# Kernel optimization log

Measured on AMD Instinct MI355X. Metric: run time of the kernel, lower is better.

## Reference

```python
import jax, jax.numpy as jnp
import numpy as np

T, B, I, H, O = 512, 64, 256, 512, 256

def setup_inputs() -> dict:
    key = jax.random.key(0)
    ks = jax.random.split(key, 7)
    s_ih = 1.0 / np.sqrt(H)
    return {
        "x": jax.random.normal(ks[0], (T, B, I), dtype=jnp.float32),
        "W_ih": jax.random.uniform(ks[1], (H, I), jnp.float32, -s_ih, s_ih),
        "W_hh": jax.random.uniform(ks[2], (H, H), jnp.float32, -s_ih, s_ih),
        "b_ih": jax.random.uniform(ks[3], (H,), jnp.float32, -s_ih, s_ih),
        "b_hh": jax.random.uniform(ks[4], (H,), jnp.float32, -s_ih, s_ih),
        "W_out": jax.random.uniform(ks[5], (O, H), jnp.float32, -s_ih, s_ih),
        "b_out": jax.random.uniform(ks[6], (O,), jnp.float32, -s_ih, s_ih),
    }

def reference(x, W_ih, W_hh, b_ih, b_hh, W_out, b_out):
    # Precompute input projection for all timesteps: [T, B, H]
    xp = jnp.einsum('tbi,hi->tbh', x, W_ih) + b_ih + b_hh

    def step(h, xp_t):
        h_new = jnp.tanh(xp_t + h @ W_hh.T)
        return h_new, h_new

    h0 = jnp.zeros((x.shape[1], W_hh.shape[0]), dtype=x.dtype)
    h_last, rnn_out = jax.lax.scan(step, h0, xp)  # rnn_out: [T, B, H]
    y = jnp.einsum('tbh,oh->tbo', rnn_out, W_out) + b_out
    return y, h_last[None]  # h: [1, B, H] matching torch nn.RNN
```

## Files before the change

### kernel.cpp

```cpp
#include <hip/hip_runtime.h>

#define T_DIM 512
#define B_DIM 64
#define I_DIM 256
#define H_DIM 512
#define O_DIM 256

typedef __attribute__((ext_vector_type(8))) short short8;
typedef __attribute__((ext_vector_type(4))) float f32x4;
typedef __attribute__((ext_vector_type(4))) int   i32x4;

__device__ __forceinline__ unsigned short f2bf(float f){
  unsigned int u = __builtin_bit_cast(unsigned int, f);
  u += 0x7fffu + ((u >> 16) & 1u);
  return (unsigned short)(u >> 16);
}
__device__ __forceinline__ float bf2f(unsigned short b){
  unsigned int u = ((unsigned int)b) << 16;
  return __builtin_bit_cast(float, u);
}

#if defined(__has_builtin)
#if __has_builtin(__builtin_amdgcn_update_dpp)
#define HAVE_DPP 1
#endif
#endif

__global__ void pack_w(const float* __restrict__ wih,
                       const float* __restrict__ wout,
                       const float* __restrict__ whh,
                       unsigned short* __restrict__ wihb,
                       unsigned short* __restrict__ woutb,
                       int* __restrict__ Wq){
  const int NW = (H_DIM*I_DIM)/4;
  int i = blockIdx.x * 256 + threadIdx.x;
  if (i < 2*NW){
    const float4* src; unsigned short* dst; int j;
    if (i < NW) { src = (const float4*)wih;  dst = wihb;  j = i; }
    else        { src = (const float4*)wout; dst = woutb; j = i - NW; }
    float4 f = src[j];
    ushort4 v;
    v.x = f2bf(f.x); v.y = f2bf(f.y); v.z = f2bf(f.z); v.w = f2bf(f.w);
    ((ushort4*)dst)[j] = v;
  } else {
    int p = i - 2*NW;
    const float s  = 0.04419417382415922f;
    const float qs = 127.0f / s;
    int out = 0;
    #pragma unroll
    for (int k = 0; k < 4; ++k){
      float w = whh[(size_t)p*4 + k];
      int q = __float2int_rn(w * qs);
      q = q < -127 ? -127 : (q > 127 ? 127 : q);
      out |= (q & 0xff) << (8*k);
    }
    Wq[p] = out;
  }
}

__global__
__attribute__((amdgpu_flat_work_group_size(512, 512), amdgpu_waves_per_eu(2, 2)))
void rnn_recur(
    const int* __restrict__ Wq,
    const unsigned short* __restrict__ xp,
    unsigned short* __restrict__ rnn,
    float* __restrict__ hlast)
{
  __shared__ union {
    char H[2][512];
    char occupancy_cap[84 * 1024];
  } sm;
  const int b    = blockIdx.x;
  const int tid  = threadIdx.x;
  const int lane = tid & 63;
  const int wv   = tid >> 6;
  const int lr   = lane & 15;
  const int hi   = lane >> 4;

  const int rloc = 16*((lane >> 2) & 3) + 4*(lane >> 4) + (lane & 3);
  const int row  = 64*wv + rloc;

  i32x4 wf[4][8];
  const char* Wb = (const char*)Wq;
  #pragma unroll
  for (int rt = 0; rt < 4; ++rt){
    const char* rowp = Wb + (size_t)(64*wv + 16*rt + lr)*512 + hi*16;
    #pragma unroll
    for (int kt = 0; kt < 8; ++kt)
      wf[rt][kt] = *(const i32x4*)(rowp + (size_t)kt*64);
  }

  if (tid < 256) ((int*)sm.H)[tid] = 0;

  const float kscale2 = 2.0f * 0.04419417382415922f / (127.0f * 127.0f);
  const int BH = B_DIM * H_DIM;

  float xp2_next = 2.0f * bf2f(xp[(size_t)b*H_DIM + row]);
  float h = 0.0f;
  __syncthreads();

  for (int t = 0; t < T_DIM; ++t){
    float xp2_cur = xp2_next;
    {
      int tn = (t + 1 < T_DIM) ? (t + 1) : t;
      xp2_next = 2.0f * bf2f(xp[(size_t)tn*BH + (size_t)b*H_DIM + row]);
    }

    const char* Hc = sm.H[t & 1];
    i32x4 bf0 = *(const i32x4*)(Hc + 0*64 + hi*16);
    i32x4 bf1 = *(const i32x4*)(Hc + 1*64 + hi*16);
    i32x4 bf2 = *(const i32x4*)(Hc + 2*64 + hi*16);
    i32x4 bf3 = *(const i32x4*)(Hc + 3*64 + hi*16);
    i32x4 bf4 = *(const i32x4*)(Hc + 4*64 + hi*16);
    i32x4 bf5 = *(const i32x4*)(Hc + 5*64 + hi*16);
    i32x4 bf6 = *(const i32x4*)(Hc + 6*64 + hi*16);
    i32x4 bf7 = *(const i32x4*)(Hc + 7*64 + hi*16);

    i32x4 a0 = {0,0,0,0}, a1 = {0,0,0,0}, a2 = {0,0,0,0}, a3 = {0,0,0,0};
    a0 = __builtin_amdgcn_mfma_i32_16x16x64_i8(wf[0][0], bf0, a0, 0, 0, 0);
    a1 = __builtin_amdgcn_mfma_i32_16x16x64_i8(wf[1][0], bf0, a1, 0, 0, 0);
    a2 = __builtin_amdgcn_mfma_i32_16x16x64_i8(wf[2][0], bf0, a2, 0, 0, 0);
    a3 = __builtin_amdgcn_mfma_i32_16x16x64_i8(wf[3][0], bf0, a3, 0, 0, 0);
    a0 = __builtin_amdgcn_mfma_i32_16x16x64_i8(wf[0][1], bf1, a0, 0, 0, 0);
    a1 = __builtin_amdgcn_mfma_i32_16x16x64_i8(wf[1][1], bf1, a1, 0, 0, 0);
    a2 = __builtin_amdgcn_mfma_i32_16x16x64_i8(wf[2][1], bf1, a2, 0, 0, 0);
    a3 = __builtin_amdgcn_mfma_i32_16x16x64_i8(wf[3][1], bf1, a3, 0, 0, 0);
    a0 = __builtin_amdgcn_mfma_i32_16x16x64_i8(wf[0][2], bf2, a0, 0, 0, 0);
    a1 = __builtin_amdgcn_mfma_i32_16x16x64_i8(wf[1][2], bf2, a1, 0, 0, 0);
    a2 = __builtin_amdgcn_mfma_i32_16x16x64_i8(wf[2][2], bf2, a2, 0, 0, 0);
    a3 = __builtin_amdgcn_mfma_i32_16x16x64_i8(wf[3][2], bf2, a3, 0, 0, 0);
    a0 = __builtin_amdgcn_mfma_i32_16x16x64_i8(wf[0][3], bf3, a0, 0, 0, 0);
    a1 = __builtin_amdgcn_mfma_i32_16x16x64_i8(wf[1][3], bf3, a1, 0, 0, 0);
    a2 = __builtin_amdgcn_mfma_i32_16x16x64_i8(wf[2][3], bf3, a2, 0, 0, 0);
    a3 = __builtin_amdgcn_mfma_i32_16x16x64_i8(wf[3][3], bf3, a3, 0, 0, 0);
    a0 = __builtin_amdgcn_mfma_i32_16x16x64_i8(wf[0][4], bf4, a0, 0, 0, 0);
    a1 = __builtin_amdgcn_mfma_i32_16x16x64_i8(wf[1][4], bf4, a1, 0, 0, 0);
    a2 = __builtin_amdgcn_mfma_i32_16x16x64_i8(wf[2][4], bf4, a2, 0, 0, 0);
    a3 = __builtin_amdgcn_mfma_i32_16x16x64_i8(wf[3][4], bf4, a3, 0, 0, 0);
    a0 = __builtin_amdgcn_mfma_i32_16x16x64_i8(wf[0][5], bf5, a0, 0, 0, 0);
    a1 = __builtin_amdgcn_mfma_i32_16x16x64_i8(wf[1][5], bf5, a1, 0, 0, 0);
    a2 = __builtin_amdgcn_mfma_i32_16x16x64_i8(wf[2][5], bf5, a2, 0, 0, 0);
    a3 = __builtin_amdgcn_mfma_i32_16x16x64_i8(wf[3][5], bf5, a3, 0, 0, 0);
    a0 = __builtin_amdgcn_mfma_i32_16x16x64_i8(wf[0][6], bf6, a0, 0, 0, 0);
    a1 = __builtin_amdgcn_mfma_i32_16x16x64_i8(wf[1][6], bf6, a1, 0, 0, 0);
    a2 = __builtin_amdgcn_mfma_i32_16x16x64_i8(wf[2][6], bf6, a2, 0, 0, 0);
    a3 = __builtin_amdgcn_mfma_i32_16x16x64_i8(wf[3][6], bf6, a3, 0, 0, 0);
    a0 = __builtin_amdgcn_mfma_i32_16x16x64_i8(wf[0][7], bf7, a0, 0, 0, 0);
    a1 = __builtin_amdgcn_mfma_i32_16x16x64_i8(wf[1][7], bf7, a1, 0, 0, 0);
    a2 = __builtin_amdgcn_mfma_i32_16x16x64_i8(wf[2][7], bf7, a2, 0, 0, 0);
    a3 = __builtin_amdgcn_mfma_i32_16x16x64_i8(wf[3][7], bf7, a3, 0, 0, 0);

    int f0, f1, f2, f3;
    {
      int e0 = (lane & 4) ? a1[0] : a0[0];
      int e1 = (lane & 4) ? a3[0] : a2[0];
      f0 = (lane & 8) ? e1 : e0;
      e0 = (lane & 4) ? a1[1] : a0[1];
      e1 = (lane & 4) ? a3[1] : a2[1];
      f1 = (lane & 8) ? e1 : e0;
      e0 = (lane & 4) ? a1[2] : a0[2];
      e1 = (lane & 4) ? a3[2] : a2[2];
      f2 = (lane & 8) ? e1 : e0;
      e0 = (lane & 4) ? a1[3] : a0[3];
      e1 = (lane & 4) ? a3[3] : a2[3];
      f3 = (lane & 8) ? e1 : e0;
    }
    int g0 = (lane & 1) ? f1 : f0;
    int g1 = (lane & 1) ? f3 : f2;
    int am = (lane & 2) ? g1 : g0;

    float pre2 = xp2_cur + (float)am * kscale2;
    float e2 = __expf(pre2);
    float rc = __builtin_amdgcn_rcpf(e2 + 1.0f);
    h = fmaf(-2.0f, rc, 1.0f);

    int q = __float2int_rn(h * 127.0f) & 0xff;
#ifdef HAVE_DPP
    int p1 = __builtin_amdgcn_update_dpp(0, q, 0xB1, 0xf, 0xf, true);
    int y  = q | (p1 << 8);
    int p2 = __builtin_amdgcn_update_dpp(0, y, 0x4E, 0xf, 0xf, true);
    int z  = y | (p2 << 16);
    if ((lane & 3) == 0) ((int*)sm.H[(t + 1) & 1])[row >> 2] = z;
#else
    sm.H[(t + 1) & 1][row] = (char)q;
#endif
    asm volatile("s_waitcnt lgkmcnt(0)" ::: "memory");
    __builtin_amdgcn_s_barrier();

    rnn[(size_t)t*BH + (size_t)b*H_DIM + row] = f2bf(h);
  }
  hlast[(size_t)b*H_DIM + row] = h;
}

template<typename TA, typename TO>
__global__ __launch_bounds__(256) void gemm_bt128(
    const TA* __restrict__ A, const unsigned short* __restrict__ B,
    TO* __restrict__ C,
    const float* __restrict__ bias1, const float* __restrict__ bias2,
    int M, int N, int K)
{
  __shared__ unsigned short As[128][40];
  __shared__ unsigned short Bs[128][40];
  const int tid  = threadIdx.x;
  const int lane = tid & 63, wid = tid >> 6;
  const int m0   = blockIdx.y * 128;
  const int n0   = blockIdx.x * 128;
  const int wm   = wid >> 1, wn = wid & 1;
  const int lr   = lane & 15, lq = lane >> 4;
  const int sr0  = tid >> 2, so = tid & 3;
  const int sr1  = 64 + sr0;

  f32x4 acc[4][4];
  #pragma unroll
  for (int i = 0; i < 4; ++i)
    #pragma unroll
    for (int j = 0; j < 4; ++j) acc[i][j] = (f32x4){0.f, 0.f, 0.f, 0.f};

  for (int k0 = 0; k0 < K; k0 += 32){
    #pragma unroll
    for (int half = 0; half < 2; ++half){
      int sr = half ? sr1 : sr0;
      const TA* src = A + (size_t)(m0 + sr)*K + k0 + so*8;
      uint4 v;
      if constexpr (__is_same(TA, float)){
        float4 q0 = *(const float4*)src;
        float4 q1 = *(const float4*)(src + 4);
        v.x = (unsigned)f2bf(q0.x) | ((unsigned)f2bf(q0.y) << 16);
        v.y = (unsigned)f2bf(q0.z) | ((unsigned)f2bf(q0.w) << 16);
        v.z = (unsigned)f2bf(q1.x) | ((unsigned)f2bf(q1.y) << 16);
        v.w = (unsigned)f2bf(q1.z) | ((unsigned)f2bf(q1.w) << 16);
      } else {
        v = *(const uint4*)src;
      }
      *(uint4*)&As[sr][so*8] = v;
    }
    *(uint4*)&Bs[sr0][so*8] = *(const uint4*)(B + (size_t)(n0 + sr0)*K + k0 + so*8);
    *(uint4*)&Bs[sr1][so*8] = *(const uint4*)(B + (size_t)(n0 + sr1)*K + k0 + so*8);
    __syncthreads();
    short8 a[4], bfr[4];
    #pragma unroll
    for (int i = 0; i < 4; ++i){
      a[i]   = __builtin_bit_cast(short8, *(const uint4*)&As[wm*64 + i*16 + lr][lq*8]);
      bfr[i] = __builtin_bit_cast(short8, *(const uint4*)&Bs[wn*64 + i*16 + lr][lq*8]);
    }
    #pragma unroll
    for (int i = 0; i < 4; ++i)
      #pragma unroll
      for (int j = 0; j < 4; ++j)
        acc[i][j] = __builtin_amdgcn_mfma_f32_16x16x32_bf16(a[i], bfr[j], acc[i][j], 0, 0, 0);
    __syncthreads();
  }

  #pragma unroll
  for (int i = 0; i < 4; ++i)
    #pragma unroll
    for (int j = 0; j < 4; ++j)
      #pragma unroll
      for (int r = 0; r < 4; ++r){
        int grow = m0 + wm*64 + i*16 + lq*4 + r;
        int gcol = n0 + wn*64 + j*16 + lr;
        float v = acc[i][j][r] + bias1[gcol];
        if (bias2) v += bias2[gcol];
        if constexpr (__is_same(TO, float)) C[(size_t)grow*N + gcol] = v;
        else                                C[(size_t)grow*N + gcol] = f2bf(v);
      }
}

extern "C" void kernel_launch(void* const* d_in, const int* in_sizes, int n_in,
                              void* d_out, int out_size, void* d_ws, size_t ws_size,
                              hipStream_t stream){
  (void)in_sizes; (void)n_in; (void)out_size; (void)ws_size;
  const float* x    = (const float*)d_in[0];
  const float* Wih  = (const float*)d_in[1];
  const float* Whh  = (const float*)d_in[2];
  const float* bih  = (const float*)d_in[3];
  const float* bhh  = (const float*)d_in[4];
  const float* Wout = (const float*)d_in[5];
  const float* bout = (const float*)d_in[6];
  float* y     = (float*)d_out;
  float* hlast = y + (size_t)T_DIM * B_DIM * O_DIM;

  char* ws = (char*)d_ws;
  const size_t MB = 1024*1024;
  unsigned short* xp   = (unsigned short*)ws;
  unsigned short* rnn  = (unsigned short*)(ws + 32*MB);
  int*            Wq   = (int*)           (ws + 64*MB);
  unsigned short* wob  = (unsigned short*)(ws + 64*MB + 256*1024);
  unsigned short* wihb = (unsigned short*)(ws + 64*MB + 512*1024);

  pack_w<<<512, 256, 0, stream>>>(Wih, Wout, Whh, wihb, wob, Wq);
  gemm_bt128<float, unsigned short><<<dim3(4, 256), 256, 0, stream>>>(
      x, wihb, xp, bih, bhh, T_DIM*B_DIM, H_DIM, I_DIM);
  rnn_recur<<<64, 512, 0, stream>>>(Wq, xp, rnn, hlast);
  gemm_bt128<unsigned short, float><<<dim3(2, 256), 256, 0, stream>>>(
      rnn, wob, y, bout, nullptr, T_DIM*B_DIM, O_DIM, H_DIM);
}
```

Baseline: 497.5 us.

## Fuse output GEMM into recurrence kernel with progress-flag producer/consumer overlap

```diff
diff --git a/kernel.cpp b/kernel.cpp
--- a/kernel.cpp
+++ b/kernel.cpp
@@ -6,6 +6,9 @@
 #define H_DIM 512
 #define O_DIM 256
 
+#define RNN_BLOCKS 64
+#define G2_BLOCKS  128
+
 typedef __attribute__((ext_vector_type(8))) short short8;
 typedef __attribute__((ext_vector_type(4))) float f32x4;
 typedef __attribute__((ext_vector_type(4))) int   i32x4;
@@ -31,9 +34,11 @@
                        const float* __restrict__ whh,
                        unsigned short* __restrict__ wihb,
                        unsigned short* __restrict__ woutb,
-                       int* __restrict__ Wq){
+                       int* __restrict__ Wq,
+                       int* __restrict__ prog){
   const int NW = (H_DIM*I_DIM)/4;
   int i = blockIdx.x * 256 + threadIdx.x;
+  if (blockIdx.x == 0 && threadIdx.x < B_DIM) prog[threadIdx.x] = 0;
   if (i < 2*NW){
     const float4* src; unsigned short* dst; int j;
     if (i < NW) { src = (const float4*)wih;  dst = wihb;  j = i; }
@@ -60,136 +65,207 @@
 
 __global__
 __attribute__((amdgpu_flat_work_group_size(512, 512), amdgpu_waves_per_eu(2, 2)))
-void rnn_recur(
+void rnn_gemm2(
     const int* __restrict__ Wq,
     const unsigned short* __restrict__ xp,
     unsigned short* __restrict__ rnn,
-    float* __restrict__ hlast)
+    float* __restrict__ hlast,
+    const unsigned short* __restrict__ wob,
+    const float* __restrict__ bout,
+    float* __restrict__ y,
+    int* __restrict__ prog)
 {
   __shared__ union {
     char H[2][512];
+    struct { unsigned short As[128][40]; unsigned short Bs[128][40]; } g;
     char occupancy_cap[84 * 1024];
   } sm;
-  const int b    = blockIdx.x;
-  const int tid  = threadIdx.x;
+  const int blk = blockIdx.x;
+  const int tid = threadIdx.x;
   const int lane = tid & 63;
-  const int wv   = tid >> 6;
-  const int lr   = lane & 15;
-  const int hi   = lane >> 4;
-
-  const int rloc = 16*((lane >> 2) & 3) + 4*(lane >> 4) + (lane & 3);
-  const int row  = 64*wv + rloc;
-
-  i32x4 wf[4][8];
-  const char* Wb = (const char*)Wq;
-  #pragma unroll
-  for (int rt = 0; rt < 4; ++rt){
-    const char* rowp = Wb + (size_t)(64*wv + 16*rt + lr)*512 + hi*16;
-    #pragma unroll
-    for (int kt = 0; kt < 8; ++kt)
-      wf[rt][kt] = *(const i32x4*)(rowp + (size_t)kt*64);
+
+  if (blk < RNN_BLOCKS){
+    const int b    = blk;
+    const int wv   = tid >> 6;
+    const int lr   = lane & 15;
+    const int hi   = lane >> 4;
+    const int rloc = 16*((lane >> 2) & 3) + 4*(lane >> 4) + (lane & 3);
+    const int row  = 64*wv + rloc;
+
+    i32x4 wf[4][8];
+    const char* Wb = (const char*)Wq;
+    #pragma unroll
+    for (int rt = 0; rt < 4; ++rt){
+      const char* rowp = Wb + (size_t)(64*wv + 16*rt + lr)*512 + hi*16;
+      #pragma unroll
+      for (int kt = 0; kt < 8; ++kt)
+        wf[rt][kt] = *(const i32x4*)(rowp + (size_t)kt*64);
+    }
+
+    if (tid < 256) ((int*)sm.H)[tid] = 0;
+
+    const float kscale2 = 2.0f * 0.04419417382415922f / (127.0f * 127.0f);
+    const int BH = B_DIM * H_DIM;
+
+    float xp2_next = 2.0f * bf2f(xp[(size_t)b*H_DIM + row]);
+    float h = 0.0f;
+    __syncthreads();
+
+    for (int t = 0; t < T_DIM; ++t){
+      float xp2_cur = xp2_next;
+      {
+        int tn = (t + 1 < T_DIM) ? (t + 1) : t;
+        xp2_next = 2.0f * bf2f(xp[(size_t)tn*BH + (size_t)b*H_DIM + row]);
+      }
+
+      const char* Hc = sm.H[t & 1];
+      i32x4 bf0 = *(const i32x4*)(Hc + 0*64 + hi*16);
+      i32x4 bf1 = *(const i32x4*)(Hc + 1*64 + hi*16);
+      i32x4 bf2 = *(const i32x4*)(Hc + 2*64 + hi*16);
+      i32x4 bf3 = *(const i32x4*)(Hc + 3*64 + hi*16);
+      i32x4 bf4 = *(const i32x4*)(Hc + 4*64 + hi*16);
+      i32x4 bf5 = *(const i32x4*)(Hc + 5*64 + hi*16);
+      i32x4 bf6 = *(const i32x4*)(Hc + 6*64 + hi*16);
+      i32x4 bf7 = *(const i32x4*)(Hc + 7*64 + hi*16);
+
+      i32x4 a0 = {0,0,0,0}, a1 = {0,0,0,0}, a2 = {0,0,0,0}, a3 = {0,0,0,0};
+      a0 = __builtin_amdgcn_mfma_i32_16x16x64_i8(wf[0][0], bf0, a0, 0, 0, 0);
+      a1 = __builtin_amdgcn_mfma_i32_16x16x64_i8(wf[1][0], bf0, a1, 0, 0, 0);
+      a2 = __builtin_amdgcn_mfma_i32_16x16x64_i8(wf[2][0], bf0, a2, 0, 0, 0);
+      a3 = __builtin_amdgcn_mfma_i32_16x16x64_i8(wf[3][0], bf0, a3, 0, 0, 0);
+      a0 = __builtin_amdgcn_mfma_i32_16x16x64_i8(wf[0][1], bf1, a0, 0, 0, 0);
+      a1 = __builtin_amdgcn_mfma_i32_16x16x64_i8(wf[1][1], bf1, a1, 0, 0, 0);
+      a2 = __builtin_amdgcn_mfma_i32_16x16x64_i8(wf[2][1], bf1, a2, 0, 0, 0);
+      a3 = __builtin_amdgcn_mfma_i32_16x16x64_i8(wf[3][1], bf1, a3, 0, 0, 0);
+      a0 = __builtin_amdgcn_mfma_i32_16x16x64_i8(wf[0][2], bf2, a0, 0, 0, 0);
+      a1 = __builtin_amdgcn_mfma_i32_16x16x64_i8(wf[1][2], bf2, a1, 0, 0, 0);
+      a2 = __builtin_amdgcn_mfma_i32_16x16x64_i8(wf[2][2], bf2, a2, 0, 0, 0);
+      a3 = __builtin_amdgcn_mfma_i32_16x16x64_i8(wf[3][2], bf2, a3, 0, 0, 0);
+      a0 = __builtin_amdgcn_mfma_i32_16x16x64_i8(wf[0][3], bf3, a0, 0, 0, 0);
+      a1 = __builtin_amdgcn_mfma_i32_16x16x64_i8(wf[1][3], bf3, a1, 0, 0, 0);
+      a2 = __builtin_amdgcn_mfma_i32_16x16x64_i8(wf[2][3], bf3, a2, 0, 0, 0);
+      a3 = __builtin_amdgcn_mfma_i32_16x16x64_i8(wf[3][3], bf3, a3, 0, 0, 0);
+      a0 = __builtin_amdgcn_mfma_i32_16x16x64_i8(wf[0][4], bf4, a0, 0, 0, 0);
+      a1 = __builtin_amdgcn_mfma_i32_16x16x64_i8(wf[1][4], bf4, a1, 0, 0, 0);
+      a2 = __builtin_amdgcn_mfma_i32_16x16x64_i8(wf[2][4], bf4, a2, 0, 0, 0);
+      a3 = __builtin_amdgcn_mfma_i32_16x16x64_i8(wf[3][4], bf4, a3, 0, 0, 0);
+      a0 = __builtin_amdgcn_mfma_i32_16x16x64_i8(wf[0][5], bf5, a0, 0, 0, 0);
+      a1 = __builtin_amdgcn_mfma_i32_16x16x64_i8(wf[1][5], bf5, a1, 0, 0, 0);
+      a2 = __builtin_amdgcn_mfma_i32_16x16x64_i8(wf[2][5], bf5, a2, 0, 0, 0);
+      a3 = __builtin_amdgcn_mfma_i32_16x16x64_i8(wf[3][5], bf5, a3, 0, 0, 0);
+      a0 = __builtin_amdgcn_mfma_i32_16x16x64_i8(wf[0][6], bf6, a0, 0, 0, 0);
+      a1 = __builtin_amdgcn_mfma_i32_16x16x64_i8(wf[1][6], bf6, a1, 0, 0, 0);
+      a2 = __builtin_amdgcn_mfma_i32_16x16x64_i8(wf[2][6], bf6, a2, 0, 0, 0);
+      a3 = __builtin_amdgcn_mfma_i32_16x16x64_i8(wf[3][6], bf6, a3, 0, 0, 0);
+      a0 = __builtin_amdgcn_mfma_i32_16x16x64_i8(wf[0][7], bf7, a0, 0, 0, 0);
+      a1 = __builtin_amdgcn_mfma_i32_16x16x64_i8(wf[1][7], bf7, a1, 0, 0, 0);
+      a2 = __builtin_amdgcn_mfma_i32_16x16x64_i8(wf[2][7], bf7, a2, 0, 0, 0);
+      a3 = __builtin_amdgcn_mfma_i32_16x16x64_i8(wf[3][7], bf7, a3, 0, 0, 0);
+
+      int f0, f1, f2, f3;
+      {
+        int e0 = (lane & 4) ? a1[0] : a0[0];
+        int e1 = (lane & 4) ? a3[0] : a2[0];
+        f0 = (lane & 8) ? e1 : e0;
+        e0 = (lane & 4) ? a1[1] : a0[1];
+        e1 = (lane & 4) ? a3[1] : a2[1];
+        f1 = (lane & 8) ? e1 : e0;
+        e0 = (lane & 4) ? a1[2] : a0[2];
+        e1 = (lane & 4) ? a3[2] : a2[2];
+        f2 = (lane & 8) ? e1 : e0;
+        e0 = (lane & 4) ? a1[3] : a0[3];
+        e1 = (lane & 4) ? a3[3] : a2[3];
+        f3 = (lane & 8) ? e1 : e0;
+      }
+      int g0 = (lane & 1) ? f1 : f0;
+      int g1 = (lane & 1) ? f3 : f2;
+      int am = (lane & 2) ? g1 : g0;
+
+      float pre2 = xp2_cur + (float)am * kscale2;
+      float e2 = __expf(pre2);
+      float rc = __builtin_amdgcn_rcpf(e2 + 1.0f);
+      h = fmaf(-2.0f, rc, 1.0f);
+
+      int q = __float2int_rn(h * 127.0f) & 0xff;
+#ifdef HAVE_DPP
+      int p1 = __builtin_amdgcn_update_dpp(0, q, 0xB1, 0xf, 0xf, true);
+      int yb = q | (p1 << 8);
+      int p2 = __builtin_amdgcn_update_dpp(0, yb, 0x4E, 0xf, 0xf, true);
+      int z  = yb | (p2 << 16);
+      if ((lane & 3) == 0) ((int*)sm.H[(t + 1) & 1])[row >> 2] = z;
+#else
+      sm.H[(t + 1) & 1][row] = (char)q;
+#endif
+      asm volatile("s_waitcnt lgkmcnt(0)" ::: "memory");
+      __builtin_amdgcn_s_barrier();
+
+      rnn[(size_t)t*BH + (size_t)b*H_DIM + row] = f2bf(h);
+
+      if ((t & 7) == 7){
+        __syncthreads();
+        if (tid == 0){ __threadfence(); atomicExch(&prog[b], t + 1); }
+      }
+    }
+    hlast[(size_t)b*H_DIM + row] = h;
+
+  } else {
+    const int k2  = blk - RNN_BLOCKS;
+    const int n0  = (k2 & 1) * 128;
+    const int mb  = k2 >> 1;
+    const int wid = tid >> 6;
+    const int wm  = wid >> 2, wn = wid & 3;
+    const int lr  = lane & 15, lq = lane >> 4;
+    const int sr  = tid >> 2, so = tid & 3;
+    const int K   = H_DIM, N = O_DIM;
+
+    for (int it = 0; it < 4; ++it){
+      const int mt = mb*4 + it;
+      const int m0 = mt * 128;
+      const int need = 2*mt + 2;
+      if (tid == 0){
+        for (int pb = 0; pb < B_DIM; ++pb)
+          while (atomicAdd(&prog[pb], 0) < need) __builtin_amdgcn_s_sleep(8);
+      }
+      __syncthreads();
+      __threadfence();
+
+      f32x4 acc[4][2];
+      #pragma unroll
+      for (int i = 0; i < 4; ++i)
+        #pragma unroll
+        for (int j = 0; j < 2; ++j) acc[i][j] = (f32x4){0.f, 0.f, 0.f, 0.f};
+
+      for (int k0 = 0; k0 < K; k0 += 32){
+        *(uint4*)&sm.g.As[sr][so*8] = *(const uint4*)(rnn + (size_t)(m0 + sr)*K + k0 + so*8);
+        *(uint4*)&sm.g.Bs[sr][so*8] = *(const uint4*)(wob + (size_t)(n0 + sr)*K + k0 + so*8);
+        __syncthreads();
+        short8 a[4], bw[2];
+        #pragma unroll
+        for (int i = 0; i < 4; ++i)
+          a[i]  = __builtin_bit_cast(short8, *(const uint4*)&sm.g.As[wm*64 + i*16 + lr][lq*8]);
+        #pragma unroll
+        for (int j = 0; j < 2; ++j)
+          bw[j] = __builtin_bit_cast(short8, *(const uint4*)&sm.g.Bs[wn*32 + j*16 + lr][lq*8]);
+        #pragma unroll
+        for (int i = 0; i < 4; ++i)
+          #pragma unroll
+          for (int j = 0; j < 2; ++j)
+            acc[i][j] = __builtin_amdgcn_mfma_f32_16x16x32_bf16(a[i], bw[j], acc[i][j], 0, 0, 0);
+        __syncthreads();
+      }
+
+      #pragma unroll
+      for (int i = 0; i < 4; ++i)
+        #pragma unroll
+        for (int j = 0; j < 2; ++j)
+          #pragma unroll
+          for (int r = 0; r < 4; ++r){
+            int grow = m0 + wm*64 + i*16 + lq*4 + r;
+            int gcol = n0 + wn*32 + j*16 + lr;
+            y[(size_t)grow*N + gcol] = acc[i][j][r] + bout[gcol];
+          }
+    }
   }
-
-  if (tid < 256) ((int*)sm.H)[tid] = 0;
-
-  const float kscale2 = 2.0f * 0.04419417382415922f / (127.0f * 127.0f);
-  const int BH = B_DIM * H_DIM;
-
-  float xp2_next = 2.0f * bf2f(xp[(size_t)b*H_DIM + row]);
-  float h = 0.0f;
-  __syncthreads();
-
-  for (int t = 0; t < T_DIM; ++t){
-    float xp2_cur = xp2_next;
-    {
-      int tn = (t + 1 < T_DIM) ? (t + 1) : t;
-      xp2_next = 2.0f * bf2f(xp[(size_t)tn*BH + (size_t)b*H_DIM + row]);
-    }
-
-    const char* Hc = sm.H[t & 1];
-    i32x4 bf0 = *(const i32x4*)(Hc + 0*64 + hi*16);
-    i32x4 bf1 = *(const i32x4*)(Hc + 1*64 + hi*16);
-    i32x4 bf2 = *(const i32x4*)(Hc + 2*64 + hi*16);
-    i32x4 bf3 = *(const i32x4*)(Hc + 3*64 + hi*16);
-    i32x4 bf4 = *(const i32x4*)(Hc + 4*64 + hi*16);
-    i32x4 bf5 = *(const i32x4*)(Hc + 5*64 + hi*16);
-    i32x4 bf6 = *(const i32x4*)(Hc + 6*64 + hi*16);
-    i32x4 bf7 = *(const i32x4*)(Hc + 7*64 + hi*16);
-
-    i32x4 a0 = {0,0,0,0}, a1 = {0,0,0,0}, a2 = {0,0,0,0}, a3 = {0,0,0,0};
-    a0 = __builtin_amdgcn_mfma_i32_16x16x64_i8(wf[0][0], bf0, a0, 0, 0, 0);
-    a1 = __builtin_amdgcn_mfma_i32_16x16x64_i8(wf[1][0], bf0, a1, 0, 0, 0);
-    a2 = __builtin_amdgcn_mfma_i32_16x16x64_i8(wf[2][0], bf0, a2, 0, 0, 0);
-    a3 = __builtin_amdgcn_mfma_i32_16x16x64_i8(wf[3][0], bf0, a3, 0, 0, 0);
-    a0 = __builtin_amdgcn_mfma_i32_16x16x64_i8(wf[0][1], bf1, a0, 0, 0, 0);
-    a1 = __builtin_amdgcn_mfma_i32_16x16x64_i8(wf[1][1], bf1, a1, 0, 0, 0);
-    a2 = __builtin_amdgcn_mfma_i32_16x16x64_i8(wf[2][1], bf1, a2, 0, 0, 0);
-    a3 = __builtin_amdgcn_mfma_i32_16x16x64_i8(wf[3][1], bf1, a3, 0, 0, 0);
-    a0 = __builtin_amdgcn_mfma_i32_16x16x64_i8(wf[0][2], bf2, a0, 0, 0, 0);
-    a1 = __builtin_amdgcn_mfma_i32_16x16x64_i8(wf[1][2], bf2, a1, 0, 0, 0);
-    a2 = __builtin_amdgcn_mfma_i32_16x16x64_i8(wf[2][2], bf2, a2, 0, 0, 0);
-    a3 = __builtin_amdgcn_mfma_i32_16x16x64_i8(wf[3][2], bf2, a3, 0, 0, 0);
-    a0 = __builtin_amdgcn_mfma_i32_16x16x64_i8(wf[0][3], bf3, a0, 0, 0, 0);
-    a1 = __builtin_amdgcn_mfma_i32_16x16x64_i8(wf[1][3], bf3, a1, 0, 0, 0);
-    a2 = __builtin_amdgcn_mfma_i32_16x16x64_i8(wf[2][3], bf3, a2, 0, 0, 0);
-    a3 = __builtin_amdgcn_mfma_i32_16x16x64_i8(wf[3][3], bf3, a3, 0, 0, 0);
-    a0 = __builtin_amdgcn_mfma_i32_16x16x64_i8(wf[0][4], bf4, a0, 0, 0, 0);
-    a1 = __builtin_amdgcn_mfma_i32_16x16x64_i8(wf[1][4], bf4, a1, 0, 0, 0);
-    a2 = __builtin_amdgcn_mfma_i32_16x16x64_i8(wf[2][4], bf4, a2, 0, 0, 0);
-    a3 = __builtin_amdgcn_mfma_i32_16x16x64_i8(wf[3][4], bf4, a3, 0, 0, 0);
-    a0 = __builtin_amdgcn_mfma_i32_16x16x64_i8(wf[0][5], bf5, a0, 0, 0, 0);
-    a1 = __builtin_amdgcn_mfma_i32_16x16x64_i8(wf[1][5], bf5, a1, 0, 0, 0);
-    a2 = __builtin_amdgcn_mfma_i32_16x16x64_i8(wf[2][5], bf5, a2, 0, 0, 0);
-    a3 = __builtin_amdgcn_mfma_i32_16x16x64_i8(wf[3][5], bf5, a3, 0, 0, 0);
-    a0 = __builtin_amdgcn_mfma_i32_16x16x64_i8(wf[0][6], bf6, a0, 0, 0, 0);
-    a1 = __builtin_amdgcn_mfma_i32_16x16x64_i8(wf[1][6], bf6, a1, 0, 0, 0);
-    a2 = __builtin_amdgcn_mfma_i32_16x16x64_i8(wf[2][6], bf6, a2, 0, 0, 0);
-    a3 = __builtin_amdgcn_mfma_i32_16x16x64_i8(wf[3][6], bf6, a3, 0, 0, 0);
-    a0 = __builtin_amdgcn_mfma_i32_16x16x64_i8(wf[0][7], bf7, a0, 0, 0, 0);
-    a1 = __builtin_amdgcn_mfma_i32_16x16x64_i8(wf[1][7], bf7, a1, 0, 0, 0);
-    a2 = __builtin_amdgcn_mfma_i32_16x16x64_i8(wf[2][7], bf7, a2, 0, 0, 0);
-    a3 = __builtin_amdgcn_mfma_i32_16x16x64_i8(wf[3][7], bf7, a3, 0, 0, 0);
-
-    int f0, f1, f2, f3;
-    {
-      int e0 = (lane & 4) ? a1[0] : a0[0];
-      int e1 = (lane & 4) ? a3[0] : a2[0];
-      f0 = (lane & 8) ? e1 : e0;
-      e0 = (lane & 4) ? a1[1] : a0[1];
-      e1 = (lane & 4) ? a3[1] : a2[1];
-      f1 = (lane & 8) ? e1 : e0;
-      e0 = (lane & 4) ? a1[2] : a0[2];
-      e1 = (lane & 4) ? a3[2] : a2[2];
-      f2 = (lane & 8) ? e1 : e0;
-      e0 = (lane & 4) ? a1[3] : a0[3];
-      e1 = (lane & 4) ? a3[3] : a2[3];
-      f3 = (lane & 8) ? e1 : e0;
-    }
-    int g0 = (lane & 1) ? f1 : f0;
-    int g1 = (lane & 1) ? f3 : f2;
-    int am = (lane & 2) ? g1 : g0;
-
-    float pre2 = xp2_cur + (float)am * kscale2;
-    float e2 = __expf(pre2);
-    float rc = __builtin_amdgcn_rcpf(e2 + 1.0f);
-    h = fmaf(-2.0f, rc, 1.0f);
-
-    int q = __float2int_rn(h * 127.0f) & 0xff;
-#ifdef HAVE_DPP
-    int p1 = __builtin_amdgcn_update_dpp(0, q, 0xB1, 0xf, 0xf, true);
-    int y  = q | (p1 << 8);
-    int p2 = __builtin_amdgcn_update_dpp(0, y, 0x4E, 0xf, 0xf, true);
-    int z  = y | (p2 << 16);
-    if ((lane & 3) == 0) ((int*)sm.H[(t + 1) & 1])[row >> 2] = z;
-#else
-    sm.H[(t + 1) & 1][row] = (char)q;
-#endif
-    asm volatile("s_waitcnt lgkmcnt(0)" ::: "memory");
-    __builtin_amdgcn_s_barrier();
-
-    rnn[(size_t)t*BH + (size_t)b*H_DIM + row] = f2bf(h);
-  }
-  hlast[(size_t)b*H_DIM + row] = h;
 }
 
 template<typename TA, typename TO>
@@ -287,11 +363,11 @@
   int*            Wq   = (int*)           (ws + 64*MB);
   unsigned short* wob  = (unsigned short*)(ws + 64*MB + 256*1024);
   unsigned short* wihb = (unsigned short*)(ws + 64*MB + 512*1024);
-
-  pack_w<<<512, 256, 0, stream>>>(Wih, Wout, Whh, wihb, wob, Wq);
+  int*            prog = (int*)           (ws + 66*MB);
+
+  pack_w<<<512, 256, 0, stream>>>(Wih, Wout, Whh, wihb, wob, Wq, prog);
   gemm_bt128<float, unsigned short><<<dim3(4, 256), 256, 0, stream>>>(
       x, wihb, xp, bih, bhh, T_DIM*B_DIM, H_DIM, I_DIM);
-  rnn_recur<<<64, 512, 0, stream>>>(Wq, xp, rnn, hlast);
-  gemm_bt128<unsigned short, float><<<dim3(2, 256), 256, 0, stream>>>(
-      rnn, wob, y, bout, nullptr, T_DIM*B_DIM, O_DIM, H_DIM);
-}
+  rnn_gemm2<<<RNN_BLOCKS + G2_BLOCKS, 512, 0, stream>>>(
+      Wq, xp, rnn, hlast, wob, bout, y, prog);
+}
```

Result: slower. 653.7 us (+31.4%).
